# Kernel optimization log

Hardware: AMD Instinct MI355X
Metric: run time of the kernel (lower is better)

## Reference

```python
import jax, jax.numpy as jnp
import numpy as np

NUM_HEAD = 8


def setup_inputs() -> dict:
    key = jax.random.key(0)
    k1, k2, k3, k4 = jax.random.split(key, 4)
    B, C, H, W = 16, 512, 64, 64
    x = jax.random.normal(k1, (B, C, H, W), dtype=jnp.float32)
    w_qkv = jax.random.normal(k2, (3 * C, C), dtype=jnp.float32) * 0.02  # Conv2d 1x1, no bias
    w_proj = jax.random.normal(k3, (C, C), dtype=jnp.float32) * 0.02
    b_proj = jax.random.normal(k4, (C,), dtype=jnp.float32) * 0.02
    return {"x": x, "w_qkv": w_qkv, "w_proj": w_proj, "b_proj": b_proj}


def reference(x, w_qkv, w_proj, b_proj):
    B, C, H, W = x.shape
    nh = NUM_HEAD
    hd = C // nh
    scale = hd ** (-0.5)
    # 1x1 conv == channel matmul
    qkv = jnp.einsum('oc,bchw->bohw', w_qkv, x)  # [B, 3C, H, W]
    q, k, v = jnp.split(qkv, 3, axis=1)
    q = q.reshape(B, nh, hd, H * W)
    k = k.reshape(B, nh, hd, H * W)
    v = v.reshape(B, nh, hd, H * W)
    # NOTE: faithful to source: contracts over the spatial (last) axis,
    # producing a [B, nh, hd, hd] matrix.
    attn = jnp.einsum('bnqd,bnkd->bnqk', q, k) * scale
    attn = jax.nn.softmax(attn, axis=-1)
    # Faithful to source: 'k' and 'v' are both summed independently (outer sum),
    # exactly as torch.einsum computes it.
    out = jnp.einsum('bnqk,bnvd->bnqd', attn, v)
    out = out.reshape(B, C, H, W)
    return jnp.einsum('oc,bchw->bohw', w_proj, out) + b_proj[None, :, None, None]
```

## Files before the change

### kernel.cpp

```cpp
#include <hip/hip_runtime.h>

#define CDIM 512
#define NH 8
#define HWDIM 4096
#define TILE 128
#define NT 512

typedef float f32x2 __attribute__((ext_vector_type(2)));

__global__ __launch_bounds__(256) void prep_kernel(
    const float* __restrict__ wqkv, const float* __restrict__ wproj,
    float* __restrict__ wvT, float* __restrict__ wp) {
  int idx = blockIdx.x * 256 + threadIdx.x;
  if (idx < 4096) {
    int c = idx >> 3, n = idx & 7;
    const float* p = wqkv + (size_t)(1024 + n * 64) * CDIM + c;
    float s = 0.f;
#pragma unroll 8
    for (int j = 0; j < 64; ++j) s += p[(size_t)j * CDIM];
    wvT[idx] = s;
  } else if (idx < 8192) {
    int i2 = idx - 4096;
    int o = i2 >> 3, n = i2 & 7;
    const float* p = wproj + (size_t)o * CDIM + n * 64;
    float s = 0.f;
#pragma unroll 8
    for (int j = 0; j < 64; ++j) s += p[j];
    wp[i2] = s;
  }
}

__global__ __launch_bounds__(NT, 4) void fused_kernel(
    const float* __restrict__ x, const float* __restrict__ bias,
    const float* __restrict__ wvT, const float* __restrict__ wp,
    float* __restrict__ y) {
  __shared__ __align__(16) float sWv[4096];
  __shared__ __align__(16) float sWp[4096];
  __shared__ __align__(16) float sB[512];
  __shared__ __align__(16) float sS[8][NH][TILE];

  const int t = threadIdx.x;
  for (int i = t; i < 4096; i += NT) { sWv[i] = wvT[i]; sWp[i] = wp[i]; }
  if (t < 512) sB[t] = bias[t];
  __syncthreads();

  const int wave = t >> 6;
  const int lane = t & 63;
  const int pos0 = blockIdx.x * TILE;
  const int b = pos0 >> 12;
  const int hw0 = pos0 & (HWDIM - 1);
  const float* xb = x + ((size_t)b * CDIM) * HWDIM + hw0 + lane * 2;

  float acc[NH][2];
#pragma unroll
  for (int n = 0; n < NH; ++n) { acc[n][0] = 0.f; acc[n][1] = 0.f; }

  const int c0 = wave * 64;
#pragma unroll 8
  for (int cc = 0; cc < 64; ++cc) {
    const int c = c0 + cc;
    const float2 xv = *(const float2*)(xb + (size_t)c * HWDIM);
    const float4 w0 = *(const float4*)&sWv[c * 8];
    const float4 w1 = *(const float4*)&sWv[c * 8 + 4];
    const float wn[8] = {w0.x, w0.y, w0.z, w0.w, w1.x, w1.y, w1.z, w1.w};
#pragma unroll
    for (int n = 0; n < NH; ++n) {
      acc[n][0] = fmaf(wn[n], xv.x, acc[n][0]);
      acc[n][1] = fmaf(wn[n], xv.y, acc[n][1]);
    }
  }

#pragma unroll
  for (int n = 0; n < NH; ++n) {
    *(float2*)&sS[wave][n][lane * 2] = make_float2(acc[n][0], acc[n][1]);
  }
  __syncthreads();

  float S2[NH][2];
#pragma unroll
  for (int n = 0; n < NH; ++n) {
    float s0 = 0.f, s1 = 0.f;
#pragma unroll
    for (int w = 0; w < 8; ++w) {
      const float2 a = *(const float2*)&sS[w][n][lane * 2];
      s0 += a.x; s1 += a.y;
    }
    S2[n][0] = s0; S2[n][1] = s1;
  }

  float* yb = y + ((size_t)b * CDIM) * HWDIM + hw0 + lane * 2;
  const int o0 = wave * 64;
#pragma unroll 4
  for (int oo = 0; oo < 64; ++oo) {
    const int o = o0 + oo;
    const float4 w0 = *(const float4*)&sWp[o * 8];
    const float4 w1 = *(const float4*)&sWp[o * 8 + 4];
    const float wn[8] = {w0.x, w0.y, w0.z, w0.w, w1.x, w1.y, w1.z, w1.w};
    const float bb = sB[o];
    float r0 = bb, r1 = bb;
#pragma unroll
    for (int n = 0; n < NH; ++n) {
      r0 = fmaf(wn[n], S2[n][0], r0);
      r1 = fmaf(wn[n], S2[n][1], r1);
    }
    f32x2 out;
    out.x = r0; out.y = r1;
    __builtin_nontemporal_store(out, (f32x2*)(yb + (size_t)o * HWDIM));
  }
}

extern "C" void kernel_launch(void* const* d_in, const int* in_sizes, int n_in,
                              void* d_out, int out_size, void* d_ws, size_t ws_size,
                              hipStream_t stream) {
  const float* x     = (const float*)d_in[0];
  const float* wqkv  = (const float*)d_in[1];
  const float* wproj = (const float*)d_in[2];
  const float* bproj = (const float*)d_in[3];
  float* y = (float*)d_out;

  float* wvT = (float*)d_ws;
  float* wp  = wvT + 4096;

  prep_kernel<<<32, 256, 0, stream>>>(wqkv, wproj, wvT, wp);
  fused_kernel<<<HWDIM * 16 / TILE, NT, 0, stream>>>(x, bproj, wvT, wp, y);
}
```

Baseline: 248.3 us.

## Split fused kernel into partial-sum, reduce, and projection kernels via workspace

Replaces the single fused kernel with three kernels when the workspace is large enough. The first computes per-channel-chunk partial head sums into a workspace with wider float4 loads and register-batched x reads. The second reduces the eight partials, and the third applies the projection and bias with float4 nontemporal stores. The aim is more memory-level parallelism and wider accesses, at the cost of extra global round trips for the intermediates and two more launches. The old fused path is kept as a fallback.

```diff
diff --git a/kernel.cpp b/kernel.cpp
--- a/kernel.cpp
+++ b/kernel.cpp
@@ -3,10 +3,15 @@
 #define CDIM 512
 #define NH 8
 #define HWDIM 4096
-#define TILE 128
-#define NT 512
 
 typedef float f32x2 __attribute__((ext_vector_type(2)));
+typedef float f32x4 __attribute__((ext_vector_type(4)));
+
+#define WS_WVT 0
+#define WS_WP 4096
+#define WS_SP 8192
+#define WS_S (8192 + 8 * 16 * NH * HWDIM)
+#define WS_NEEDED_BYTES ((size_t)(8192 + 8 * 16 * NH * HWDIM + 16 * NH * HWDIM) * 4)
 
 __global__ __launch_bounds__(256) void prep_kernel(
     const float* __restrict__ wqkv, const float* __restrict__ wproj,
@@ -30,6 +35,116 @@
   }
 }
 
+
+__global__ __launch_bounds__(512) void sA_kernel(
+    const float* __restrict__ x, const float* __restrict__ wvT,
+    float* __restrict__ Sp) {
+  __shared__ float sWv[512];
+
+  const int t = threadIdx.x;
+  const int bid = blockIdx.x;
+  const int b = bid >> 4;
+  const int k = (bid >> 1) & 7;
+  const int h = bid & 1;
+  const int c0 = k * 64;
+
+  sWv[t] = wvT[c0 * 8 + t];
+  __syncthreads();
+
+  const int pos = h * 2048 + t * 4;
+  const float* xb = x + ((size_t)(b * CDIM + c0)) * HWDIM + pos;
+
+  float acc[NH][4];
+#pragma unroll
+  for (int n = 0; n < NH; ++n) { acc[n][0] = acc[n][1] = acc[n][2] = acc[n][3] = 0.f; }
+
+  for (int g = 0; g < 8; ++g) {
+    float4 xv[8];
+#pragma unroll
+    for (int j = 0; j < 8; ++j)
+      xv[j] = *(const float4*)(xb + (size_t)(g * 8 + j) * HWDIM);
+#pragma unroll
+    for (int j = 0; j < 8; ++j) {
+      const int c = g * 8 + j;
+      const float4 w0 = *(const float4*)&sWv[c * 8];
+      const float4 w1 = *(const float4*)&sWv[c * 8 + 4];
+      const float wn[8] = {w0.x, w0.y, w0.z, w0.w, w1.x, w1.y, w1.z, w1.w};
+      const float xr[4] = {xv[j].x, xv[j].y, xv[j].z, xv[j].w};
+#pragma unroll
+      for (int n = 0; n < NH; ++n) {
+#pragma unroll
+        for (int p = 0; p < 4; ++p) acc[n][p] = fmaf(wn[n], xr[p], acc[n][p]);
+      }
+    }
+  }
+
+  float* sp = Sp + ((size_t)(k * 16 + b) * NH) * HWDIM + pos;
+#pragma unroll
+  for (int n = 0; n < NH; ++n)
+    *(float4*)(sp + (size_t)n * HWDIM) = make_float4(acc[n][0], acc[n][1], acc[n][2], acc[n][3]);
+}
+
+__global__ __launch_bounds__(512) void sR_kernel(
+    const float* __restrict__ Sp, float* __restrict__ S) {
+  const size_t fid = (size_t)blockIdx.x * 512 + threadIdx.x;
+  const size_t base = fid * 4;
+  float4 s = make_float4(0.f, 0.f, 0.f, 0.f);
+#pragma unroll
+  for (int k = 0; k < 8; ++k) {
+    const float4 a = *(const float4*)(Sp + base + (size_t)k * 16 * NH * HWDIM);
+    s.x += a.x; s.y += a.y; s.z += a.z; s.w += a.w;
+  }
+  *(float4*)(S + base) = s;
+}
+
+__global__ __launch_bounds__(256) void yK_kernel(
+    const float* __restrict__ S, const float* __restrict__ wp,
+    const float* __restrict__ bias, float* __restrict__ y) {
+  __shared__ float sWp[4096];
+  __shared__ float sB[512];
+
+  const int t = threadIdx.x;
+  for (int i = t; i < 4096; i += 256) sWp[i] = wp[i];
+  for (int i = t; i < 512; i += 256) sB[i] = bias[i];
+  __syncthreads();
+
+  const int bid = blockIdx.x;
+  const int b = bid >> 5;
+  const int span = (bid >> 3) & 3;
+  const int og = bid & 7;
+  const int hwo = span * 1024 + t * 4;
+
+  float s[NH][4];
+#pragma unroll
+  for (int n = 0; n < NH; ++n) {
+    const float4 a = *(const float4*)&S[((size_t)b * NH + n) * HWDIM + hwo];
+    s[n][0] = a.x; s[n][1] = a.y; s[n][2] = a.z; s[n][3] = a.w;
+  }
+
+  float* yb = y + ((size_t)b * CDIM) * HWDIM + hwo;
+  const int o0 = og * 64;
+#pragma unroll 4
+  for (int oo = 0; oo < 64; ++oo) {
+    const int o = o0 + oo;
+    const float4 w0 = *(const float4*)&sWp[o * 8];
+    const float4 w1 = *(const float4*)&sWp[o * 8 + 4];
+    const float wn[8] = {w0.x, w0.y, w0.z, w0.w, w1.x, w1.y, w1.z, w1.w};
+    const float bb = sB[o];
+    f32x4 r;
+    r.x = bb; r.y = bb; r.z = bb; r.w = bb;
+#pragma unroll
+    for (int n = 0; n < NH; ++n) {
+      r.x = fmaf(wn[n], s[n][0], r.x);
+      r.y = fmaf(wn[n], s[n][1], r.y);
+      r.z = fmaf(wn[n], s[n][2], r.z);
+      r.w = fmaf(wn[n], s[n][3], r.w);
+    }
+    __builtin_nontemporal_store(r, (f32x4*)(yb + (size_t)o * HWDIM));
+  }
+}
+
+#define TILE 128
+#define NT 512
 __global__ __launch_bounds__(NT, 4) void fused_kernel(
     const float* __restrict__ x, const float* __restrict__ bias,
     const float* __restrict__ wvT, const float* __restrict__ wp,
@@ -69,11 +184,9 @@
       acc[n][1] = fmaf(wn[n], xv.y, acc[n][1]);
     }
   }
-
-#pragma unroll
-  for (int n = 0; n < NH; ++n) {
+#pragma unroll
+  for (int n = 0; n < NH; ++n)
     *(float2*)&sS[wave][n][lane * 2] = make_float2(acc[n][0], acc[n][1]);
-  }
   __syncthreads();
 
   float S2[NH][2];
@@ -118,9 +231,18 @@
   const float* bproj = (const float*)d_in[3];
   float* y = (float*)d_out;
 
-  float* wvT = (float*)d_ws;
-  float* wp  = wvT + 4096;
+  float* wvT = (float*)d_ws + WS_WVT;
+  float* wp  = (float*)d_ws + WS_WP;
 
   prep_kernel<<<32, 256, 0, stream>>>(wqkv, wproj, wvT, wp);
-  fused_kernel<<<HWDIM * 16 / TILE, NT, 0, stream>>>(x, bproj, wvT, wp, y);
-}
+
+  if (ws_size >= WS_NEEDED_BYTES) {
+    float* Sp = (float*)d_ws + WS_SP;
+    float* S  = (float*)d_ws + WS_S;
+    sA_kernel<<<256, 512, 0, stream>>>(x, wvT, Sp);
+    sR_kernel<<<256, 512, 0, stream>>>(Sp, S);
+    yK_kernel<<<512, 256, 0, stream>>>(S, wp, bproj, y);
+  } else {
+    fused_kernel<<<HWDIM * 16 / TILE, NT, 0, stream>>>(x, bproj, wvT, wp, y);
+  }
+}
```

Result: slower. 256.2 us (+3.2%).
